# Performance work log

Hardware: AMD Instinct MI355X
Metric: run time of the kernel (lower is better)

The kernel has to match this reference:

```python
import jax, jax.numpy as jnp
import numpy as np

B, D, U, HU = 2048, 1024, 1024, 256

def _ln(x, eps=1e-3):
    # Keras LayerNormalization(center=False, scale=False), default epsilon=1e-3
    m = jnp.mean(x, axis=-1, keepdims=True)
    v = jnp.var(x, axis=-1, keepdims=True)
    return (x - m) * jax.lax.rsqrt(v + eps)

def setup_inputs() -> dict:
    key = jax.random.key(0)
    ks = jax.random.split(key, 17)
    s = 0.02
    return {
        "inputs": jax.random.normal(ks[0], (B, D), jnp.float32),
        "main_h": 0.1 * jax.random.normal(ks[1], (B, U), jnp.float32),
        "main_c": 0.1 * jax.random.normal(ks[2], (B, U), jnp.float32),
        "hyper_h": 0.1 * jax.random.normal(ks[3], (B, HU), jnp.float32),
        "hyper_c": 0.1 * jax.random.normal(ks[4], (B, HU), jnp.float32),
        "kernel": s * jax.random.normal(ks[5], (D, 4 * U), jnp.float32),
        "recurrent_kernel": s * jax.random.normal(ks[6], (U, 4 * U), jnp.float32),
        "bias": jnp.zeros((4 * U,), jnp.float32),
        "hyper_kernel": s * jax.random.normal(ks[7], (D + U, 4 * HU), jnp.float32),
        "hyper_rec_kernel": s * jax.random.normal(ks[8], (HU, 4 * HU), jnp.float32),
        "hyper_bias": jnp.zeros((4 * HU,), jnp.float32),
        "dx_w": s * jax.random.normal(ks[9], (HU, 4 * U), jnp.float32),
        "dx_b": s * jax.random.normal(ks[10], (4 * U,), jnp.float32),
        "dh_w": s * jax.random.normal(ks[11], (HU, 4 * U), jnp.float32),
        "dh_b": s * jax.random.normal(ks[12], (4 * U,), jnp.float32),
        "db_w": s * jax.random.normal(ks[13], (HU, 4 * U), jnp.float32),
        "db_b": s * jax.random.normal(ks[14], (4 * U,), jnp.float32),
    }

def reference(inputs, main_h, main_c, hyper_h, hyper_c,
              kernel, recurrent_kernel, bias,
              hyper_kernel, hyper_rec_kernel, hyper_bias,
              dx_w, dx_b, dh_w, dh_b, db_w, db_b):
    # --- hyper LSTMCell (Keras gate order i, f, g, o) ---
    hx = jnp.concatenate([inputs, main_h], axis=-1)          # [B, D+U]
    z = hx @ hyper_kernel + hyper_h @ hyper_rec_kernel + hyper_bias  # [B, 4*HU]
    hi, hf, hg, ho = jnp.split(z, 4, axis=-1)
    hyper_c_new = jax.nn.sigmoid(hf) * hyper_c + jax.nn.sigmoid(hi) * jnp.tanh(hg)
    hyper_out = jax.nn.sigmoid(ho) * jnp.tanh(hyper_c_new)  # = hyper_h_new

    # --- hypernet gate scalings ---
    d_x = hyper_out @ dx_w + dx_b                            # [B, 4*U]
    d_h = hyper_out @ dh_w + dh_b
    d_b = hyper_out @ db_w + db_b

    # --- main LSTM gates with hyper modulation + LayerNorm ---
    proj_x = inputs @ kernel + bias                          # [B, 4*U]
    proj_h = main_h @ recurrent_kernel                       # [B, 4*U]
    gates = _ln(d_x * proj_x + d_h * proj_h + d_b)
    i, f, g, o = jnp.split(gates, 4, axis=-1)
    main_c_new = jax.nn.sigmoid(f) * main_c + jax.nn.sigmoid(i) * jnp.tanh(g)
    main_h_new = jax.nn.sigmoid(o) * jnp.tanh(_ln(main_c_new))
    return (main_h_new, main_c_new, hyper_out, hyper_c_new)
```

## Files before the change

### kernel.cpp

```cpp
#include <hip/hip_runtime.h>
#include <cstdint>

typedef unsigned short u16;
typedef _Float16 half8 __attribute__((ext_vector_type(8)));
typedef float floatx4 __attribute__((ext_vector_type(4)));
typedef unsigned short ushort8v __attribute__((ext_vector_type(8)));
typedef unsigned short ushort4v __attribute__((ext_vector_type(4)));
typedef float float4v __attribute__((ext_vector_type(4)));

#define BB 2048
#define UU 1024
#define HUx 256
#define O_H  0
#define O_C  (BB*UU)
#define O_HO (2*BB*UU)
#define O_HC (2*BB*UU + BB*HUx)
#define MFMAH __builtin_amdgcn_mfma_f32_16x16x32_f16

#define LBAR() do { \
    asm volatile("s_waitcnt lgkmcnt(0)\n\ts_barrier" ::: "memory"); \
    __builtin_amdgcn_sched_barrier(0); \
} while (0)

__device__ __forceinline__ float bf2f(u16 u) {
    union { uint32_t i; float f; } v; v.i = ((uint32_t)u) << 16; return v.f;
}
__device__ __forceinline__ u16 f2bf(float f) {
    union { float f; uint32_t i; } v; v.f = f;
    uint32_t r = v.i + 0x7fffu + ((v.i >> 16) & 1u);
    return (u16)(r >> 16);
}
__device__ __forceinline__ u16 f2h(float f) {
    _Float16 h = (_Float16)f; u16 u; __builtin_memcpy(&u, &h, 2); return u;
}
__device__ __forceinline__ float sigf(float x) { return 1.f / (1.f + expf(-x)); }
__device__ __forceinline__ float ldmix(const void* p, size_t i, int isbf) {
    return isbf ? bf2f(((const u16*)p)[i]) : ((const float*)p)[i];
}
__device__ __forceinline__ u16 ld2h(const void* p, size_t i, int isbf) {
    return f2h(ldmix(p, i, isbf));
}

__device__ __forceinline__ void ld128(half8 r[2], const u16* src, int row0, int ldK,
                                      int k0, int tid) {
    #pragma unroll
    for (int i = 0; i < 2; i++) {
        int v = tid + 256 * i;
        r[i] = *(const half8*)(src + (size_t)(row0 + (v >> 2)) * ldK + k0 + (v & 3) * 8);
    }
}
__device__ __forceinline__ void ld64(half8& r, const u16* src, int row0, int ldK,
                                     int k0, int tid) {
    r = *(const half8*)(src + (size_t)(row0 + (tid >> 2)) * ldK + k0 + (tid & 3) * 8);
}
__device__ __forceinline__ void wr128(u16* lds, const half8 r[2], int tid) {
    #pragma unroll
    for (int i = 0; i < 2; i++) {
        int v = tid + 256 * i;
        *(half8*)&lds[(v >> 2) * 40 + (v & 3) * 8] = r[i];
    }
}
__device__ __forceinline__ void wr64(u16* lds, half8 r, int tid) {
    *(half8*)&lds[(tid >> 2) * 40 + (tid & 3) * 8] = r;
}
__device__ __forceinline__ void wrS128(u16* lds, const half8 r[2], int tid) {
    #pragma unroll
    for (int i = 0; i < 2; i++) {
        int v = tid + 256 * i;
        int ps = (v & 3) ^ ((v >> 3) & 3);
        *(half8*)&lds[(v >> 2) * 32 + ps * 8] = r[i];
    }
}
__device__ __forceinline__ void wrS64(u16* lds, half8 r, int tid) {
    int ps = (tid & 3) ^ ((tid >> 3) & 3);
    *(half8*)&lds[(tid >> 2) * 32 + ps * 8] = r;
}

__device__ __forceinline__ int detect_local(const u16* raw) {
    int lane = threadIdx.x & 63;
    u16 u = raw[2 * lane];
    int e = (u >> 7) & 0xFF;
    unsigned long long m = __ballot(e >= 100 && e <= 134);
    return (__popcll(m) >= 32) ? 1 : 0;
}

__device__ __forceinline__ void transpose_tile_v(const void* in, u16* out, int C,
                                                 int ostride, int ocol, int r0, int c0,
                                                 int isbf, u16* th ) {
    int tid = threadIdx.x;
    int ty = tid >> 3, tx4 = (tid & 7) * 4;
    ushort4v v;
    if (isbf) {
        ushort4v q = *(const ushort4v*)((const u16*)in + (size_t)(r0 + ty) * C + c0 + tx4);
        #pragma unroll
        for (int j = 0; j < 4; j++) v[j] = f2h(bf2f(q[j]));
    } else {
        float4v q = *(const float4v*)((const float*)in + (size_t)(r0 + ty) * C + c0 + tx4);
        #pragma unroll
        for (int j = 0; j < 4; j++) v[j] = f2h(q[j]);
    }
    *(ushort4v*)&th[ty * 36 + tx4] = v;
    __syncthreads();
    ushort4v w;
    #pragma unroll
    for (int j = 0; j < 4; j++) w[j] = th[(tx4 + j) * 36 + ty];
    *(ushort4v*)(out + (size_t)(c0 + ty) * ostride + ocol + r0 + tx4) = w;
}

__global__ __launch_bounds__(256) void prep_in(
    const void* __restrict__ xs, const void* __restrict__ ms, const void* __restrict__ hs,
    const void* __restrict__ hyper_k, const void* __restrict__ hyper_rk,
    u16* __restrict__ xh, u16* __restrict__ mh, u16* __restrict__ hh,
    u16* __restrict__ BTh, int* __restrict__ flag) {
    __shared__ __align__(16) u16 th[32 * 36];
    int bid = blockIdx.x, tid = threadIdx.x;
    int isbf = detect_local((const u16*)xs);
    if (bid == 0 && tid == 0) *flag = isbf;

    if (bid < 2304) {
        int i = bid * 256 + tid;
        const void* src; u16* dst; int t;
        if (i < 262144)      { src = xs; dst = xh; t = i; }
        else if (i < 524288) { src = ms; dst = mh; t = i - 262144; }
        else                 { src = hs; dst = hh; t = i - 524288; }
        half8 o;
        if (isbf) {
            ushort8v v = *(const ushort8v*)((const u16*)src + (size_t)t * 8);
            #pragma unroll
            for (int j = 0; j < 8; j++) o[j] = (_Float16)bf2f(v[j]);
        } else {
            float4v a = *(const float4v*)((const float*)src + (size_t)t * 8);
            float4v b = *(const float4v*)((const float*)src + (size_t)t * 8 + 4);
            #pragma unroll
            for (int j = 0; j < 4; j++) { o[j] = (_Float16)a[j]; o[j + 4] = (_Float16)b[j]; }
        }
        *(half8*)(dst + (size_t)t * 8) = o;
    } else if (bid < 4352) {
        int u = bid - 2304;
        transpose_tile_v(hyper_k, BTh, 1024, 2304, 0, (u >> 5) * 32, (u & 31) * 32, isbf, th);
    } else {
        int u = bid - 4352;
        transpose_tile_v(hyper_rk, BTh, 1024, 2304, 2048, (u >> 5) * 32, (u & 31) * 32, isbf, th);
    }
}

__device__ __forceinline__ void gh_load(half8 pA[2], half8& pB,
                                        const u16* xh, const u16* mh, const u16* hh,
                                        const u16* BT, int bm, int bn, int s, int tid) {
    const u16* Ap; int ldA, kA;
    if (s < 32)      { Ap = xh; ldA = 1024; kA = s * 32; }
    else if (s < 64) { Ap = mh; ldA = 1024; kA = (s - 32) * 32; }
    else             { Ap = hh; ldA = 256;  kA = (s - 64) * 32; }
    ld128(pA, Ap, bm, ldA, kA, tid);
    ld64(pB, BT, bn, 2304, s * 32, tid);
}

__global__ __launch_bounds__(256) void gemm_hyper_wt(
    const u16* __restrict__ xh, const u16* __restrict__ mh, const u16* __restrict__ hh,
    const u16* __restrict__ BT, float* __restrict__ z,
    const void* __restrict__ xs,
    const void* __restrict__ kernel_w, const void* __restrict__ rec_w,
    const void* __restrict__ dx_w, const void* __restrict__ dh_w,
    const void* __restrict__ db_w,
    u16* __restrict__ kT, u16* __restrict__ rkT,
    u16* __restrict__ dxT, u16* __restrict__ dhT, u16* __restrict__ dbT) {
    __shared__ __align__(16) u16 sA[128 * 40];
    __shared__ __align__(16) u16 sB[64 * 40];
    int bid = blockIdx.x, tid = threadIdx.x;

    if (bid >= 512) {
        int isbf = detect_local((const u16*)xs);
        int u = bid - 512;
        const void* in; u16* out; int ostride, r0, c0;
        if (u < 8192) {
            in  = (u < 4096) ? kernel_w : rec_w;
            out = (u < 4096) ? kT : rkT;
            int r = u & 4095;
            ostride = 1024; r0 = (r >> 7) * 32; c0 = (r & 127) * 32;
        } else {
            int v = u - 8192;
            int zi = v >> 10, r = v & 1023;
            in  = (zi == 0) ? dx_w : (zi == 1) ? dh_w : db_w;
            out = (zi == 0) ? dxT : (zi == 1) ? dhT : dbT;
            ostride = 256; r0 = (r >> 7) * 32; c0 = (r & 127) * 32;
        }
        transpose_tile_v(in, out, 4096, ostride, 0, r0, c0, isbf, sA);
        return;
    }

    int bxv = bid & 15, byv = (bid >> 4) & 15, bzv = bid >> 8;
    int lane = tid & 63, wave = tid >> 6;
    int wm = (wave & 1) * 64, wn = (wave >> 1) * 32;
    int bm = byv * 128, bn = bxv * 64;
    int s0 = bzv * 36, s1 = s0 + 36;
    floatx4 acc[4][2] = {};
    int mr = lane & 15, kq = (lane >> 4) * 8;

    half8 pA[2]; half8 pB;
    gh_load(pA, pB, xh, mh, hh, BT, bm, bn, s0, tid);
    wr128(sA, pA, tid); wr64(sB, pB, tid);
    gh_load(pA, pB, xh, mh, hh, BT, bm, bn, s0 + 1, tid);
    LBAR();

    #pragma unroll 1
    for (int s = s0; s < s1; s++) {
        half8 a[4], b[2];
        #pragma unroll
        for (int t = 0; t < 4; t++) a[t] = *(const half8*)&sA[(wm + t * 16 + mr) * 40 + kq];
        #pragma unroll
        for (int t = 0; t < 2; t++) b[t] = *(const half8*)&sB[(wn + t * 16 + mr) * 40 + kq];
        #pragma unroll
        for (int tm = 0; tm < 4; tm++)
            #pragma unroll
            for (int tn = 0; tn < 2; tn++)
                acc[tm][tn] = MFMAH(a[tm], b[tn], acc[tm][tn], 0, 0, 0);
        LBAR();
        if (s < s1 - 1) {
            wr128(sA, pA, tid); wr64(sB, pB, tid);
            if (s < s1 - 2)
                gh_load(pA, pB, xh, mh, hh, BT, bm, bn, s + 2, tid);
            LBAR();
        }
    }

    float* zp = z + (size_t)bzv * 2048 * 1024;
    #pragma unroll
    for (int tm = 0; tm < 4; tm++)
        #pragma unroll
        for (int tn = 0; tn < 2; tn++) {
            int col = bn + wn + tn * 16 + (lane & 15);
            #pragma unroll
            for (int rr = 0; rr < 4; rr++) {
                int row = bm + wm + tm * 16 + (lane >> 4) * 4 + rr;
                zp[(size_t)row * 1024 + col] = acc[tm][tn][rr];
            }
        }
}

__global__ void hyper_cell(const float* __restrict__ z, const void* __restrict__ hyper_c,
                           const void* __restrict__ hyper_bias, void* __restrict__ out,
                           u16* __restrict__ ho16, const int* __restrict__ flag) {
    int isbf = *flag;
    int t = blockIdx.x * 256 + threadIdx.x;
    int k = t & 255;
    const float* zr  = z + (size_t)(t >> 8) * 1024;
    const float* zr2 = zr + (size_t)2048 * 1024;
    float hi = zr[k]       + zr2[k]       + ldmix(hyper_bias, k, isbf);
    float hf = zr[k + 256] + zr2[k + 256] + ldmix(hyper_bias, k + 256, isbf);
    float hg = zr[k + 512] + zr2[k + 512] + ldmix(hyper_bias, k + 512, isbf);
    float ho = zr[k + 768] + zr2[k + 768] + ldmix(hyper_bias, k + 768, isbf);
    float c  = ldmix(hyper_c, t, isbf);
    float cn = sigf(hf) * c + sigf(hi) * tanhf(hg);
    float hout = sigf(ho) * tanhf(cn);
    ho16[t] = f2h(hout);
    if (isbf) {
        ((u16*)out)[O_HO + t] = f2bf(hout);
        ((u16*)out)[O_HC + t] = f2bf(cn);
    } else {
        ((float*)out)[O_HO + t] = hout;
        ((float*)out)[O_HC + t] = cn;
    }
}

__global__ __launch_bounds__(256, 2) void mega_fused(
    const u16* __restrict__ xh, const u16* __restrict__ mh, const u16* __restrict__ ho16,
    const u16* __restrict__ kT, const u16* __restrict__ rkT,
    const u16* __restrict__ dxT, const u16* __restrict__ dhT, const u16* __restrict__ dbT,
    const void* __restrict__ bias, const void* __restrict__ dx_b,
    const void* __restrict__ dh_b, const void* __restrict__ db_b,
    u16* __restrict__ gp, const int* __restrict__ flag) {
    __shared__ __align__(16) u16 S[2][12288];
    int isbf = *flag;
    int tid = threadIdx.x, lane = tid & 63, wave = tid >> 6;
    int wm = (wave & 1) * 64, wn = (wave >> 1) * 32;
    int bm = blockIdx.y * 128, bn = blockIdx.x * 64;
    floatx4 apx[4][2] = {}, aph[4][2] = {}, adx[4][2] = {}, adh[4][2] = {}, adb[4][2] = {};
    int mr = lane & 15;
    int kqs = (((lane >> 4) ^ ((mr >> 1) & 3))) * 8;

    half8 nA1[2], nA2[2], nB1, nB2, nB3;

    ld128(nA1, xh,  bm, 1024, 0, tid);
    ld128(nA2, mh,  bm, 1024, 0, tid);
    ld64(nB1, kT,  bn, 1024, 0, tid);
    ld64(nB2, rkT, bn, 1024, 0, tid);
    wrS128(S[0], nA1, tid); wrS128(S[0] + 4096, nA2, tid);
    wrS64(S[0] + 8192, nB1, tid); wrS64(S[0] + 10240, nB2, tid);
    ld128(nA1, xh,  bm, 1024, 32, tid);
    ld128(nA2, mh,  bm, 1024, 32, tid);
    ld64(nB1, kT,  bn, 1024, 32, tid);
    ld64(nB2, rkT, bn, 1024, 32, tid);
    LBAR();

    #pragma unroll 1
    for (int k0 = 0; k0 < 1024; k0 += 32) {
        int p = (k0 >> 5) & 1;
        const u16* C = S[p];
        u16* N = S[p ^ 1];
        half8 ax[4], am[4], bk[2], br[2];
        #pragma unroll
        for (int t = 0; t < 4; t++) {
            int ra = (wm + t * 16 + mr) * 32 + kqs;
            ax[t] = *(const half8*)&C[ra];
            am[t] = *(const half8*)&C[4096 + ra];
        }
        #pragma unroll
        for (int t = 0; t < 2; t++) {
            int rb = (wn + t * 16 + mr) * 32 + kqs;
            bk[t] = *(const half8*)&C[8192 + rb];
            br[t] = *(const half8*)&C[10240 + rb];
        }
        if (k0 < 992) {
            wrS128(N, nA1, tid); wrS128(N + 4096, nA2, tid);
            wrS64(N + 8192, nB1, tid); wrS64(N + 10240, nB2, tid);
        } else {
            wrS128(N, nA1, tid);
            wrS64(N + 8192, nB1, tid); wrS64(N + 10240, nB2, tid); wrS64(N + 4096, nB3, tid);
        }
        if (k0 < 960) {
            ld128(nA1, xh,  bm, 1024, k0 + 64, tid);
            ld128(nA2, mh,  bm, 1024, k0 + 64, tid);
            ld64(nB1, kT,  bn, 1024, k0 + 64, tid);
            ld64(nB2, rkT, bn, 1024, k0 + 64, tid);
        } else if (k0 == 960) {
            ld128(nA1, ho16, bm, 256, 0, tid);
            ld64(nB1, dxT, bn, 256, 0, tid);
            ld64(nB2, dhT, bn, 256, 0, tid);
            ld64(nB3, dbT, bn, 256, 0, tid);
        } else {
            ld128(nA1, ho16, bm, 256, 32, tid);
            ld64(nB1, dxT, bn, 256, 32, tid);
            ld64(nB2, dhT, bn, 256, 32, tid);
            ld64(nB3, dbT, bn, 256, 32, tid);
        }
        #pragma unroll
        for (int tm = 0; tm < 4; tm++)
            #pragma unroll
            for (int tn = 0; tn < 2; tn++) {
                apx[tm][tn] = MFMAH(ax[tm], bk[tn], apx[tm][tn], 0, 0, 0);
                aph[tm][tn] = MFMAH(am[tm], br[tn], aph[tm][tn], 0, 0, 0);
            }
        LBAR();
    }

    #pragma unroll 1
    for (int k0 = 0; k0 < 256; k0 += 32) {
        int p = (k0 >> 5) & 1;
        const u16* C = S[p];
        u16* N = S[p ^ 1];
        half8 a[4], bx[2], bh[2], bb[2];
        #pragma unroll
        for (int t = 0; t < 4; t++) {
            int ra = (wm + t * 16 + mr) * 32 + kqs;
            a[t] = *(const half8*)&C[ra];
        }
        #pragma unroll
        for (int t = 0; t < 2; t++) {
            int rb = (wn + t * 16 + mr) * 32 + kqs;
            bx[t] = *(const half8*)&C[8192 + rb];
            bh[t] = *(const half8*)&C[10240 + rb];
            bb[t] = *(const half8*)&C[4096 + rb];
        }
        if (k0 < 224) {
            wrS128(N, nA1, tid);
            wrS64(N + 8192, nB1, tid); wrS64(N + 10240, nB2, tid); wrS64(N + 4096, nB3, tid);
        }
        if (k0 < 192) {
            ld128(nA1, ho16, bm, 256, k0 + 64, tid);
            ld64(nB1, dxT, bn, 256, k0 + 64, tid);
            ld64(nB2, dhT, bn, 256, k0 + 64, tid);
            ld64(nB3, dbT, bn, 256, k0 + 64, tid);
        }
        #pragma unroll
        for (int tm = 0; tm < 4; tm++)
            #pragma unroll
            for (int tn = 0; tn < 2; tn++) {
                adx[tm][tn] = MFMAH(a[tm], bx[tn], adx[tm][tn], 0, 0, 0);
                adh[tm][tn] = MFMAH(a[tm], bh[tn], adh[tm][tn], 0, 0, 0);
                adb[tm][tn] = MFMAH(a[tm], bb[tn], adb[tm][tn], 0, 0, 0);
            }
        LBAR();
    }

    #pragma unroll
    for (int tn = 0; tn < 2; tn++) {
        int col = bn + wn + tn * 16 + (lane & 15);
        float bv  = ldmix(bias, col, isbf);
        float dxb = ldmix(dx_b, col, isbf);
        float dhb = ldmix(dh_b, col, isbf);
        float dbb = ldmix(db_b, col, isbf);
        #pragma unroll
        for (int tm = 0; tm < 4; tm++) {
            #pragma unroll
            for (int rr = 0; rr < 4; rr++) {
                int row = bm + wm + tm * 16 + (lane >> 4) * 4 + rr;
                float px = apx[tm][tn][rr] + bv;
                float ph = aph[tm][tn][rr];
                float dx = adx[tm][tn][rr] + dxb;
                float dh = adh[tm][tn][rr] + dhb;
                float db = adb[tm][tn][rr] + dbb;
                gp[(size_t)row * 4096 + col] = f2h(dx * px + dh * ph + db);
            }
        }
    }
}

__device__ __forceinline__ void block_reduce2(float& a, float& b, float* red) {
    #pragma unroll
    for (int o = 32; o > 0; o >>= 1) {
        a += __shfl_down(a, o, 64);
        b += __shfl_down(b, o, 64);
    }
    int lane = threadIdx.x & 63, w = threadIdx.x >> 6;
    if (lane == 0) { red[w] = a; red[4 + w] = b; }
    __syncthreads();
    a = red[0] + red[1] + red[2] + red[3];
    b = red[4] + red[5] + red[6] + red[7];
    __syncthreads();
}

__global__ __launch_bounds__(256) void ln_main(const u16* __restrict__ gp,
                                               const void* __restrict__ main_c,
                                               void* __restrict__ out,
                                               const int* __restrict__ flag) {
    __shared__ float sPre[4096];
    __shared__ float sC[1024];
    __shared__ float red[8];
    int isbf = *flag;
    int b = blockIdx.x, tid = threadIdx.x;
    const u16* g = gp + (size_t)b * 4096;
    float s = 0.f, q = 0.f;
    for (int j0 = tid * 8; j0 < 4096; j0 += 2048) {
        half8 v = *(const half8*)(g + j0);
        #pragma unroll
        for (int e = 0; e < 8; e++) {
            float f = (float)v[e];
            sPre[j0 + e] = f; s += f; q += f * f;
        }
    }
    block_reduce2(s, q, red);
    float mean = s * (1.f / 4096.f);
    float var = q * (1.f / 4096.f) - mean * mean;
    float rs = rsqrtf(var + 1e-3f);
    float s2 = 0.f, q2 = 0.f;
    for (int u = tid; u < 1024; u += 256) {
        float gi = (sPre[u] - mean) * rs;
        float gf = (sPre[u + 1024] - mean) * rs;
        float gg = (sPre[u + 2048] - mean) * rs;
        float c = ldmix(main_c, (size_t)b * 1024 + u, isbf);
        float cn = sigf(gf) * c + sigf(gi) * tanhf(gg);
        sC[u] = cn;
        if (isbf) ((u16*)out)[O_C + (size_t)b * 1024 + u] = f2bf(cn);
        else      ((float*)out)[O_C + (size_t)b * 1024 + u] = cn;
        s2 += cn; q2 += cn * cn;
    }
    block_reduce2(s2, q2, red);
    float m2 = s2 * (1.f / 1024.f);
    float v2 = q2 * (1.f / 1024.f) - m2 * m2;
    float rs2 = rsqrtf(v2 + 1e-3f);
    for (int u = tid; u < 1024; u += 256) {
        float go = (sPre[u + 3072] - mean) * rs;
        float hn = sigf(go) * tanhf((sC[u] - m2) * rs2);
        if (isbf) ((u16*)out)[O_H + (size_t)b * 1024 + u] = f2bf(hn);
        else      ((float*)out)[O_H + (size_t)b * 1024 + u] = hn;
    }
}

extern "C" void kernel_launch(void* const* d_in, const int* in_sizes, int n_in,
                              void* d_out, int out_size, void* d_ws, size_t ws_size,
                              hipStream_t stream) {
    (void)in_sizes; (void)n_in; (void)out_size; (void)ws_size;
    const void* inputs   = d_in[0];
    const void* main_h   = d_in[1];
    const void* main_c   = d_in[2];
    const void* hyper_h  = d_in[3];
    const void* hyper_c  = d_in[4];
    const void* kernel_w = d_in[5];
    const void* rec_w    = d_in[6];
    const void* bias     = d_in[7];
    const void* hyper_k  = d_in[8];
    const void* hyper_rk = d_in[9];
    const void* hyper_b  = d_in[10];
    const void* dx_w = d_in[11];
    const void* dx_b = d_in[12];
    const void* dh_w = d_in[13];
    const void* dh_b = d_in[14];
    const void* db_w = d_in[15];
    const void* db_b = d_in[16];
    char* ws = (char*)d_ws;
    const size_t MB = 1024 * 1024;

    int* flag = (int*)ws;
    size_t off = 256;
    u16* xh  = (u16*)(ws + off); off += 4 * MB;
    u16* mh  = (u16*)(ws + off); off += 4 * MB;
    u16* hh  = (u16*)(ws + off); off += 1 * MB;
    u16* ho  = (u16*)(ws + off); off += 1 * MB;
    u16* kT  = (u16*)(ws + off); off += 8 * MB;
    u16* rkT = (u16*)(ws + off); off += 8 * MB;
    u16* dxT = (u16*)(ws + off); off += 2 * MB;
    u16* dhT = (u16*)(ws + off); off += 2 * MB;
    u16* dbT = (u16*)(ws + off); off += 2 * MB;
    u16* BTh = (u16*)(ws + off); off += (size_t)1024 * 2304 * 2;
    float* zbuf = (float*)(ws + off); off += 16 * MB;
    u16* gp    = (u16*)(ws + off); off += 16 * MB;

    prep_in<<<4608, 256, 0, stream>>>(inputs, main_h, hyper_h, hyper_k, hyper_rk,
                                      xh, mh, hh, BTh, flag);
    gemm_hyper_wt<<<12288, 256, 0, stream>>>(xh, mh, hh, BTh, zbuf, inputs,
                                             kernel_w, rec_w, dx_w, dh_w, db_w,
                                             kT, rkT, dxT, dhT, dbT);
    hyper_cell<<<2048, 256, 0, stream>>>(zbuf, hyper_c, hyper_b, d_out, ho, flag);
    mega_fused<<<dim3(64, 16), 256, 0, stream>>>(xh, mh, ho, kT, rkT, dxT, dhT, dbT,
                                                 bias, dx_b, dh_b, db_b, gp, flag);
    ln_main<<<2048, 256, 0, stream>>>(gp, main_c, d_out, flag);
}
```

Before: 259.4 us.

## Fuse hyper LSTM cell epilogue into hyper GEMM and drop split-K

Changes the hyper GEMM tile mapping so each block holds the matching i/f/g/o gate columns for 32 hidden units, which lets the LSTM cell nonlinearity run in the GEMM epilogue. This removes the fp32 z buffer write/read and the separate hyper_cell launch. Split-K is dropped and the K loop is double-buffered in swizzled LDS. Only 128 GEMM blocks now run the full K=2304, which reduces parallelism and lengthens that part's critical path, partly hidden by the concurrent weight-transpose blocks.

```diff
diff --git a/kernel.cpp b/kernel.cpp
--- a/kernel.cpp
+++ b/kernel.cpp
@@ -52,16 +52,6 @@
 __device__ __forceinline__ void ld64(half8& r, const u16* src, int row0, int ldK,
                                      int k0, int tid) {
     r = *(const half8*)(src + (size_t)(row0 + (tid >> 2)) * ldK + k0 + (tid & 3) * 8);
-}
-__device__ __forceinline__ void wr128(u16* lds, const half8 r[2], int tid) {
-    #pragma unroll
-    for (int i = 0; i < 2; i++) {
-        int v = tid + 256 * i;
-        *(half8*)&lds[(v >> 2) * 40 + (v & 3) * 8] = r[i];
-    }
-}
-__device__ __forceinline__ void wr64(u16* lds, half8 r, int tid) {
-    *(half8*)&lds[(tid >> 2) * 40 + (tid & 3) * 8] = r;
 }
 __device__ __forceinline__ void wrS128(u16* lds, const half8 r[2], int tid) {
     #pragma unroll
@@ -144,121 +134,127 @@
     }
 }
 
-__device__ __forceinline__ void gh_load(half8 pA[2], half8& pB,
-                                        const u16* xh, const u16* mh, const u16* hh,
-                                        const u16* BT, int bm, int bn, int s, int tid) {
-    const u16* Ap; int ldA, kA;
-    if (s < 32)      { Ap = xh; ldA = 1024; kA = s * 32; }
-    else if (s < 64) { Ap = mh; ldA = 1024; kA = (s - 32) * 32; }
-    else             { Ap = hh; ldA = 256;  kA = (s - 64) * 32; }
-    ld128(pA, Ap, bm, ldA, kA, tid);
-    ld64(pB, BT, bn, 2304, s * 32, tid);
-}
-
-__global__ __launch_bounds__(256) void gemm_hyper_wt(
+__global__ __launch_bounds__(256) void gemm_cell_wt(
     const u16* __restrict__ xh, const u16* __restrict__ mh, const u16* __restrict__ hh,
-    const u16* __restrict__ BT, float* __restrict__ z,
-    const void* __restrict__ xs,
+    const u16* __restrict__ BT,
+    const void* __restrict__ xs, const void* __restrict__ hyper_c,
+    const void* __restrict__ hyper_b, void* __restrict__ out, u16* __restrict__ ho16,
     const void* __restrict__ kernel_w, const void* __restrict__ rec_w,
     const void* __restrict__ dx_w, const void* __restrict__ dh_w,
     const void* __restrict__ db_w,
     u16* __restrict__ kT, u16* __restrict__ rkT,
     u16* __restrict__ dxT, u16* __restrict__ dhT, u16* __restrict__ dbT) {
-    __shared__ __align__(16) u16 sA[128 * 40];
-    __shared__ __align__(16) u16 sB[64 * 40];
+    __shared__ __align__(16) u16 S[2][8192];
     int bid = blockIdx.x, tid = threadIdx.x;
 
-    if (bid >= 512) {
+    if (bid >= 128) {
         int isbf = detect_local((const u16*)xs);
-        int u = bid - 512;
-        const void* in; u16* out; int ostride, r0, c0;
+        int u = bid - 128;
+        const void* in; u16* outT; int ostride, r0, c0;
         if (u < 8192) {
             in  = (u < 4096) ? kernel_w : rec_w;
-            out = (u < 4096) ? kT : rkT;
+            outT = (u < 4096) ? kT : rkT;
             int r = u & 4095;
             ostride = 1024; r0 = (r >> 7) * 32; c0 = (r & 127) * 32;
         } else {
             int v = u - 8192;
             int zi = v >> 10, r = v & 1023;
             in  = (zi == 0) ? dx_w : (zi == 1) ? dh_w : db_w;
-            out = (zi == 0) ? dxT : (zi == 1) ? dhT : dbT;
+            outT = (zi == 0) ? dxT : (zi == 1) ? dhT : dbT;
             ostride = 256; r0 = (r >> 7) * 32; c0 = (r & 127) * 32;
         }
-        transpose_tile_v(in, out, 4096, ostride, 0, r0, c0, isbf, sA);
+        transpose_tile_v(in, outT, 4096, ostride, 0, r0, c0, isbf, (u16*)S);
         return;
     }
 
-    int bxv = bid & 15, byv = (bid >> 4) & 15, bzv = bid >> 8;
+    int isbf = detect_local((const u16*)xs);
     int lane = tid & 63, wave = tid >> 6;
-    int wm = (wave & 1) * 64, wn = (wave >> 1) * 32;
-    int bm = byv * 128, bn = bxv * 64;
-    int s0 = bzv * 36, s1 = s0 + 36;
-    floatx4 acc[4][2] = {};
-    int mr = lane & 15, kq = (lane >> 4) * 8;
-
-    half8 pA[2]; half8 pB;
-    gh_load(pA, pB, xh, mh, hh, BT, bm, bn, s0, tid);
-    wr128(sA, pA, tid); wr64(sB, pB, tid);
-    gh_load(pA, pB, xh, mh, hh, BT, bm, bn, s0 + 1, tid);
+    int wm = (wave & 1) * 64, ws = wave >> 1;
+    int bx = bid & 7, by = bid >> 3;
+    int bm = by * 128;
+    int mr = lane & 15;
+    int kqs = ((lane >> 4) ^ ((mr >> 1) & 3)) * 8;
+    floatx4 acc[4][4] = {};
+
+    half8 nA[2], nB[2];
+
+    #define LDA_S(R, S_) do { \
+        int s_ = (S_); \
+        const u16* Ap_; int ldA_, kA_; \
+        if (s_ < 32)      { Ap_ = xh; ldA_ = 1024; kA_ = s_ * 32; } \
+        else if (s_ < 64) { Ap_ = mh; ldA_ = 1024; kA_ = (s_ - 32) * 32; } \
+        else              { Ap_ = hh; ldA_ = 256;  kA_ = (s_ - 64) * 32; } \
+        ld128(R, Ap_, bm, ldA_, kA_, tid); \
+    } while (0)
+    #define LDB_S(R, S_) do { \
+        int s_ = (S_); \
+        _Pragma("unroll") \
+        for (int i_ = 0; i_ < 2; i_++) { \
+            int v_ = tid + 256 * i_; \
+            int br_ = v_ >> 2; \
+            int col_ = ((br_ & 63) >> 4) * 256 + (bx * 2 + (br_ >> 6)) * 16 + (br_ & 15); \
+            (R)[i_] = *(const half8*)(BT + (size_t)col_ * 2304 + s_ * 32 + (v_ & 3) * 8); \
+        } \
+    } while (0)
+
+    LDA_S(nA, 0); LDB_S(nB, 0);
+    wrS128(S[0], nA, tid); wrS128(S[0] + 4096, nB, tid);
+    LDA_S(nA, 1); LDB_S(nB, 1);
     LBAR();
 
     #pragma unroll 1
-    for (int s = s0; s < s1; s++) {
-        half8 a[4], b[2];
-        #pragma unroll
-        for (int t = 0; t < 4; t++) a[t] = *(const half8*)&sA[(wm + t * 16 + mr) * 40 + kq];
-        #pragma unroll
-        for (int t = 0; t < 2; t++) b[t] = *(const half8*)&sB[(wn + t * 16 + mr) * 40 + kq];
+    for (int s = 0; s < 72; s++) {
+        int p = s & 1;
+        const u16* C = S[p];
+        u16* N = S[p ^ 1];
+        half8 a[4], b[4];
+        #pragma unroll
+        for (int t = 0; t < 4; t++)
+            a[t] = *(const half8*)&C[(wm + t * 16 + mr) * 32 + kqs];
+        #pragma unroll
+        for (int t = 0; t < 4; t++)
+            b[t] = *(const half8*)&C[4096 + (ws * 64 + t * 16 + mr) * 32 + kqs];
+        if (s < 71) {
+            wrS128(N, nA, tid); wrS128(N + 4096, nB, tid);
+            if (s < 70) { LDA_S(nA, s + 2); LDB_S(nB, s + 2); }
+        }
         #pragma unroll
         for (int tm = 0; tm < 4; tm++)
             #pragma unroll
-            for (int tn = 0; tn < 2; tn++)
+            for (int tn = 0; tn < 4; tn++)
                 acc[tm][tn] = MFMAH(a[tm], b[tn], acc[tm][tn], 0, 0, 0);
         LBAR();
-        if (s < s1 - 1) {
-            wr128(sA, pA, tid); wr64(sB, pB, tid);
-            if (s < s1 - 2)
-                gh_load(pA, pB, xh, mh, hh, BT, bm, bn, s + 2, tid);
-            LBAR();
-        }
-    }
-
-    float* zp = z + (size_t)bzv * 2048 * 1024;
+    }
+    #undef LDA_S
+    #undef LDB_S
+
+    int hu = (bx * 2 + ws) * 16 + mr;
+    float bi = ldmix(hyper_b, hu, isbf);
+    float bf = ldmix(hyper_b, hu + 256, isbf);
+    float bg = ldmix(hyper_b, hu + 512, isbf);
+    float bo = ldmix(hyper_b, hu + 768, isbf);
     #pragma unroll
-    for (int tm = 0; tm < 4; tm++)
-        #pragma unroll
-        for (int tn = 0; tn < 2; tn++) {
-            int col = bn + wn + tn * 16 + (lane & 15);
-            #pragma unroll
-            for (int rr = 0; rr < 4; rr++) {
-                int row = bm + wm + tm * 16 + (lane >> 4) * 4 + rr;
-                zp[(size_t)row * 1024 + col] = acc[tm][tn][rr];
+    for (int tm = 0; tm < 4; tm++) {
+        #pragma unroll
+        for (int rr = 0; rr < 4; rr++) {
+            int row = bm + wm + tm * 16 + (lane >> 4) * 4 + rr;
+            size_t idx = (size_t)row * 256 + hu;
+            float hi = acc[tm][0][rr] + bi;
+            float hf = acc[tm][1][rr] + bf;
+            float hg = acc[tm][2][rr] + bg;
+            float hoo = acc[tm][3][rr] + bo;
+            float c = ldmix(hyper_c, idx, isbf);
+            float cn = sigf(hf) * c + sigf(hi) * tanhf(hg);
+            float hout = sigf(hoo) * tanhf(cn);
+            ho16[idx] = f2h(hout);
+            if (isbf) {
+                ((u16*)out)[O_HO + idx] = f2bf(hout);
+                ((u16*)out)[O_HC + idx] = f2bf(cn);
+            } else {
+                ((float*)out)[O_HO + idx] = hout;
+                ((float*)out)[O_HC + idx] = cn;
             }
         }
-}
-
-__global__ void hyper_cell(const float* __restrict__ z, const void* __restrict__ hyper_c,
-                           const void* __restrict__ hyper_bias, void* __restrict__ out,
-                           u16* __restrict__ ho16, const int* __restrict__ flag) {
-    int isbf = *flag;
-    int t = blockIdx.x * 256 + threadIdx.x;
-    int k = t & 255;
-    const float* zr  = z + (size_t)(t >> 8) * 1024;
-    const float* zr2 = zr + (size_t)2048 * 1024;
-    float hi = zr[k]       + zr2[k]       + ldmix(hyper_bias, k, isbf);
-    float hf = zr[k + 256] + zr2[k + 256] + ldmix(hyper_bias, k + 256, isbf);
-    float hg = zr[k + 512] + zr2[k + 512] + ldmix(hyper_bias, k + 512, isbf);
-    float ho = zr[k + 768] + zr2[k + 768] + ldmix(hyper_bias, k + 768, isbf);
-    float c  = ldmix(hyper_c, t, isbf);
-    float cn = sigf(hf) * c + sigf(hi) * tanhf(hg);
-    float hout = sigf(ho) * tanhf(cn);
-    ho16[t] = f2h(hout);
-    if (isbf) {
-        ((u16*)out)[O_HO + t] = f2bf(hout);
-        ((u16*)out)[O_HC + t] = f2bf(cn);
-    } else {
-        ((float*)out)[O_HO + t] = hout;
-        ((float*)out)[O_HC + t] = cn;
     }
 }
 
@@ -502,15 +498,14 @@
     u16* dhT = (u16*)(ws + off); off += 2 * MB;
     u16* dbT = (u16*)(ws + off); off += 2 * MB;
     u16* BTh = (u16*)(ws + off); off += (size_t)1024 * 2304 * 2;
-    float* zbuf = (float*)(ws + off); off += 16 * MB;
-    u16* gp    = (u16*)(ws + off); off += 16 * MB;
+    u16* gp  = (u16*)(ws + off); off += 16 * MB;
 
     prep_in<<<4608, 256, 0, stream>>>(inputs, main_h, hyper_h, hyper_k, hyper_rk,
                                       xh, mh, hh, BTh, flag);
-    gemm_hyper_wt<<<12288, 256, 0, stream>>>(xh, mh, hh, BTh, zbuf, inputs,
-                                             kernel_w, rec_w, dx_w, dh_w, db_w,
-                                             kT, rkT, dxT, dhT, dbT);
-    hyper_cell<<<2048, 256, 0, stream>>>(zbuf, hyper_c, hyper_b, d_out, ho, flag);
+    gemm_cell_wt<<<128 + 11264, 256, 0, stream>>>(xh, mh, hh, BTh,
+                                                  inputs, hyper_c, hyper_b, d_out, ho,
+                                                  kernel_w, rec_w, dx_w, dh_w, db_w,
+                                                  kT, rkT, dxT, dhT, dbT);
     mega_fused<<<dim3(64, 16), 256, 0, stream>>>(xh, mh, ho, kT, rkT, dxT, dhT, dbT,
                                                  bias, dx_b, dh_b, db_b, gp, flag);
     ln_main<<<2048, 256, 0, stream>>>(gp, main_c, d_out, flag);
```

After: 271.4 us. 1.05x slower.
